# Performance work log

Hardware: AMD Instinct MI355X
Metric: run time of the kernel (lower is better)

## Reference

```python
import jax, jax.numpy as jnp
import numpy as np

PH = PW = 4      # patch_size
NH = 8           # num_heads
C = 64           # channels
AD = 256         # attention_dim
DH = AD // NH    # dim_head (used for softmax scaling)
K = 2            # n_keys
HID = 4 * C      # MBConv hidden dim (expansion_rate=4)
GROUPS = NH


def _to_patches(x):
    # 'b c (h ph) (w pw) -> b (h w) (ph pw c)'
    B, c, H, W = x.shape
    h, w = H // PH, W // PW
    x = x.reshape(B, c, h, PH, w, PW)
    return x.transpose(0, 2, 4, 3, 5, 1).reshape(B, h * w, PH * PW * c)


def _conv(x, w, b, groups, pad):
    out = jax.lax.conv_general_dilated(
        x, w, (1, 1), pad,
        dimension_numbers=('NCHW', 'OIHW', 'NCHW'),
        feature_group_count=groups)
    return out + b[None, :, None, None]


def _mbconv(x, conv1_w, conv1_b, dw_w, dw_b, se_w1, se_b1, se_w2, se_b2, conv2_w, conv2_b):
    # grouped 1x1 expansion -> depthwise 3x3 -> squeeze-excite -> grouped 1x1 projection
    h = jax.nn.gelu(_conv(x, conv1_w, conv1_b, GROUPS, 'VALID'))
    h = jax.nn.gelu(_conv(h, dw_w, dw_b, HID, [(1, 1), (1, 1)]))
    s = h.mean(axis=(2, 3))                       # (B, HID)
    s = jax.nn.silu(s @ se_w1.T + se_b1)
    s = jax.nn.sigmoid(s @ se_w2.T + se_b2)
    h = h * s[:, :, None, None]
    return _conv(h, conv2_w, conv2_b, GROUPS, 'VALID')


def setup_inputs():
    key = jax.random.key(0)
    ks = jax.random.split(key, 18)
    mk = lambda i, shape, s=1.0: jax.random.normal(ks[i], shape, jnp.float32) * s
    return dict(
        key0=mk(0, (4, C, 128, 128)),
        key1=mk(1, (4, C, 96, 96)),
        query0=mk(2, (4, C, 128, 128)),
        query1=mk(3, (4, C, 64, 64)),
        Wk=mk(4, (PH * PW * C // NH, AD), 0.05),
        bk=mk(5, (AD,), 0.02),
        Wq=mk(6, (PH * PW * C // NH, AD), 0.05),
        bq=mk(7, (AD,), 0.02),
        conv1_w=mk(8, (HID, C * NH * K // GROUPS, 1, 1), 0.05),
        conv1_b=mk(9, (HID,), 0.02),
        dw_w=mk(10, (HID, 1, 3, 3), 0.1),
        dw_b=mk(11, (HID,), 0.02),
        se_w1=mk(12, (HID // 4, HID), 0.05),
        se_b1=mk(13, (HID // 4,), 0.02),
        se_w2=mk(14, (HID, HID // 4), 0.05),
        se_b2=mk(15, (HID,), 0.02),
        conv2_w=mk(16, (C, HID // GROUPS, 1, 1), 0.05),
        conv2_b=mk(17, (C,), 0.02),
    )


def reference(key0, key1, query0, query1, Wk, bk, Wq, bq,
              conv1_w, conv1_b, dw_w, dw_b,
              se_w1, se_b1, se_w2, se_b2, conv2_w, conv2_b):
    keys = [key0, key1]
    queries = [query0, query1]
    q_sizes = [q.shape[-2:] for q in queries]
    # image dims are multiples of patch size -> pad_to_next_multiple_of is identity
    keys_p = [_to_patches(k) for k in keys]    # (B, n_i, PH*PW*C)
    qs_p = [_to_patches(q) for q in queries]
    nk = [p.shape[1] for p in keys_p]
    nq = [p.shape[1] for p in qs_p]

    to_heads = lambda x: x.reshape(x.shape[0], x.shape[1], NH, -1).transpose(0, 2, 1, 3)
    k_seq = to_heads(jnp.concatenate(keys_p, axis=1))   # (B, NH, Nk, patch_dim)
    q_seq = to_heads(jnp.concatenate(qs_p, axis=1))     # (B, NH, Nq, patch_dim)

    k_emb = k_seq @ Wk + bk    # (B, NH, Nk, AD)
    q_emb = q_seq @ Wq + bq    # (B, NH, Nq, AD)

    attn = jnp.einsum('bhid,bhjd->bhij', q_emb, k_emb)
    attn = jax.nn.softmax(attn / DH ** 0.5, axis=-1)    # (B, NH, Nq, Nk)

    # split over key sources, weight un-embedded value patches (shared across heads)
    offs = np.cumsum([0] + nk)
    wv = [jnp.einsum('bhij,bjc->bhic', attn[..., offs[i]:offs[i + 1]], keys_p[i])
          for i in range(K)]
    wv = jnp.stack(wv, axis=1)   # (B, K, NH, Nq, PH*PW*C)

    qoffs = np.cumsum([0] + nq)
    outs = []
    for i, (qh, qw) in enumerate(q_sizes):
        v = wv[:, :, :, qoffs[i]:qoffs[i + 1], :]
        B = v.shape[0]
        h, w = qh // PH, qw // PW
        # 'b k hd (h w) (ph pw c) -> b (hd k c) (h ph) (w pw)'
        v = v.reshape(B, K, NH, h, w, PH, PW, C)
        v = v.transpose(0, 2, 1, 7, 3, 5, 4, 6).reshape(B, NH * K * C, h * PH, w * PW)
        outs.append(_mbconv(v, conv1_w, conv1_b, dw_w, dw_b,
                            se_w1, se_b1, se_w2, se_b2, conv2_w, conv2_b))
    return tuple(outs)
```

## Files before the change

### kernel.cpp

```cpp
#include <hip/hip_runtime.h>
#include <hip/hip_bf16.h>

typedef __hip_bfloat16 bf16;
typedef short s8v __attribute__((ext_vector_type(8)));
typedef float f4v __attribute__((ext_vector_type(4)));

__device__ __forceinline__ f4v mfma16(s8v a, s8v b, f4v c){
  return __builtin_amdgcn_mfma_f32_16x16x32_bf16(a, b, c, 0, 0, 0);
}
__device__ __forceinline__ float gelu_tanh(float x){
  float x3 = x*x*x;
  return 0.5f*x*(1.0f + tanhf(0.7978845608028654f*(x + 0.044715f*x3)));
}

__global__ void k_fill(float* out, int n, float val){
  int i = blockIdx.x*256 + threadIdx.x;
  if (i < n) out[i] = val;
}

__global__ __launch_bounds__(256) void k_prep(const float* __restrict__ Wk, const float* __restrict__ Wq,
                       const float* __restrict__ c1wf,
                       bf16* __restrict__ Wkt, bf16* __restrict__ Wqt, bf16* __restrict__ c1w){
  int tid = blockIdx.x*256 + threadIdx.x;
  if (tid < 32768){ int d = tid >> 7, j = tid & 127; Wkt[tid] = __float2bfloat16(Wk[j*256 + d]); }
  else if (tid < 65536){ int r = tid - 32768; int d = r >> 7, j = r & 127; Wqt[r] = __float2bfloat16(Wq[j*256 + d]); }
  else { int r = tid - 65536; c1w[r] = __float2bfloat16(c1wf[r]); }
}

__global__ __launch_bounds__(256) void k_patch4(const float* __restrict__ k0, const float* __restrict__ k1,
                         const float* __restrict__ q0, const float* __restrict__ q1,
                         bf16* __restrict__ Kp, bf16* __restrict__ Qp, bf16* __restrict__ Vt){
  __shared__ float tile[64][33];
  int gy = blockIdx.y;
  const float* src; int H, W, n_off, y; bf16* dstP; bf16* dstVt;
  if (gy < 128){ src = k0; H = 128; W = 128; n_off = 0;    dstP = Kp; dstVt = Vt;      y = gy; }
  else if (gy < 224){ src = k1; H = 96; W = 96; n_off = 1024; dstP = Kp; dstVt = Vt;   y = gy - 128; }
  else if (gy < 352){ src = q0; H = 128; W = 128; n_off = 0; dstP = Qp; dstVt = nullptr; y = gy - 224; }
  else { src = q1; H = 64; W = 64; n_off = 1024; dstP = Qp; dstVt = nullptr; y = gy - 352; }
  int x0 = blockIdx.x*32;
  if (x0 >= W) return;
  int t = threadIdx.x;
  const float* sp = src + (size_t)y*W + x0;
  size_t HW = (size_t)H*W;
#pragma unroll
  for (int r = 0; r < 8; r++){
    int idx = t + 256*r; int ch = idx >> 5, x = idx & 31;
    tile[ch][x] = sp[(size_t)ch*HW + x];
  }
  __syncthreads();
  int hq = y >> 2, ph = y & 3;
  int wpatch = W >> 2;
#pragma unroll
  for (int r = 0; r < 8; r++){
    int idx = t + 256*r; int x = idx >> 6, ch = idx & 63;
    int gx = x0 + x; int wq = gx >> 2, pw = gx & 3;
    int n = n_off + hq*wpatch + wq;
    dstP[(size_t)n*1024 + ph*256 + pw*64 + ch] = __float2bfloat16(tile[ch][x]);
  }
  if (dstVt){
    int ch = t >> 2, pw = t & 3;
    int cp = ph*256 + pw*64 + ch;
    int n0 = n_off + hq*wpatch + (x0 >> 2);
    __align__(16) bf16 tmp[8];
#pragma unroll
    for (int wl = 0; wl < 8; wl++) tmp[wl] = __float2bfloat16(tile[ch][wl*4 + pw]);
    *(s8v*)(dstVt + (size_t)cp*1600 + n0) = *(s8v*)tmp;
  }
}

__global__ __launch_bounds__(256) void k_emb2(const bf16* __restrict__ Kp, const bf16* __restrict__ Qp,
                       const bf16* __restrict__ Wkt, const bf16* __restrict__ Wqt,
                       const float* __restrict__ bk, const float* __restrict__ bq,
                       bf16* __restrict__ Ke, bf16* __restrict__ Qe, float* __restrict__ St){
  if (blockIdx.x < 40) St[blockIdx.x*256 + threadIdx.x] = 0.f;
  int bx = blockIdx.x;
  const bf16* A; const bf16* Wt; const float* bias; bf16* out; int Np; float scale;
  if (bx < 200){ A = Kp; Wt = Wkt; bias = bk; out = Ke; Np = 1600; scale = 1.0f; }
  else { bx -= 200; A = Qp; Wt = Wqt; bias = bq; out = Qe; Np = 1280; scale = 0.17677669529663687f; }
  int t = threadIdx.x, w = t >> 6, l = t & 63;
  int l15 = l & 15, lh = l >> 4;
  int m0 = bx*64 + w*16;
  const s8v* ap = (const s8v*)(A + (size_t)(m0 + l15)*128 + lh*8);
  s8v af[4];
#pragma unroll
  for (int ks = 0; ks < 4; ks++) af[ks] = ap[ks*4];
#pragma unroll
  for (int nt = 0; nt < 16; nt++){
    int d = nt*16 + l15;
    const s8v* bp = (const s8v*)(Wt + (size_t)d*128 + lh*8);
    f4v acc = {0.f,0.f,0.f,0.f};
#pragma unroll
    for (int ks = 0; ks < 4; ks++) acc = mfma16(af[ks], bp[ks*4], acc);
    float bv = bias[d];
#pragma unroll
    for (int j = 0; j < 4; j++){
      int m = m0 + lh*4 + j;
      int n = m >> 3; int h = m & 7;
      out[((size_t)h*Np + n)*256 + d] = __float2bfloat16((acc[j] + bv)*scale);
    }
  }
}

__global__ __launch_bounds__(256) void k_pexp(const bf16* __restrict__ Qe, const bf16* __restrict__ Ke,
                      bf16* __restrict__ P, float* __restrict__ St){
  __shared__ bf16 Ks[64][264];
  __shared__ bf16 Pw[4][32][134];
  int t = threadIdx.x, w = t >> 6, l = t & 63, l15 = l & 15, lh = l >> 4;
  int qt = blockIdx.x, h = blockIdx.y;
  int zz2 = blockIdx.z;
  int b2 = zz2 / 5, kc = zz2 - b2*5;
  const bf16* Qeb = Qe + (size_t)b2*2621440;
  const bf16* Keb = Ke + (size_t)b2*3276800;
  bf16* Pb = P + (size_t)b2*16384000;
  float* Stb = St + (size_t)b2*10240;
  int row0 = qt*128 + w*32;
  int cb = kc*320;
  s8v qf[2][8];
#pragma unroll
  for (int rt = 0; rt < 2; rt++)
#pragma unroll
    for (int ks = 0; ks < 8; ks++)
      qf[rt][ks] = *(const s8v*)(Qeb + ((size_t)h*1280 + row0 + rt*16 + l15)*256 + ks*32 + lh*8);
  float rs0[4] = {0.f,0.f,0.f,0.f}, rs1[4] = {0.f,0.f,0.f,0.f};
  int kr = t >> 2, kq = t & 3;
  size_t prow_base = (size_t)h*1280 + row0;
  s8v kreg[8];
  {
    const bf16* s0 = Keb + ((size_t)h*1600 + kc*320 + kr)*256 + kq*64;
#pragma unroll
    for (int u = 0; u < 8; u++) kreg[u] = *(const s8v*)(s0 + u*8);
  }
  for (int i = 0; i < 5; i++){
    if (i) __syncthreads();
#pragma unroll
    for (int u = 0; u < 8; u++){
      int sw = (kq*8 + u) ^ (kr & 7);
      *(s8v*)&Ks[kr][sw*8] = kreg[u];
    }
    if (i < 4){
      const bf16* sn = Keb + ((size_t)h*1600 + kc*320 + (i+1)*64 + kr)*256 + kq*64;
#pragma unroll
      for (int u = 0; u < 8; u++) kreg[u] = *(const s8v*)(sn + u*8);
    }
    __syncthreads();
    f4v a0[4], a1[4];
#pragma unroll
    for (int ct = 0; ct < 4; ct++){ a0[ct] = (f4v){0.f,0.f,0.f,0.f}; a1[ct] = (f4v){0.f,0.f,0.f,0.f}; }
#pragma unroll
    for (int ct = 0; ct < 4; ct++){
      int krow = ct*16 + l15;
#pragma unroll
      for (int ks = 0; ks < 8; ks++){
        s8v bf = *(const s8v*)&Ks[krow][((ks*4 + lh) ^ (krow & 7))*8];
        a0[ct] = mfma16(qf[0][ks], bf, a0[ct]);
        a1[ct] = mfma16(qf[1][ks], bf, a1[ct]);
      }
    }
#pragma unroll
    for (int ct = 0; ct < 4; ct++){
      int local = (i*4 + ct) & 7;
#pragma unroll
      for (int j = 0; j < 4; j++){
        float e0 = __expf(a0[ct][j]); rs0[j] += e0;
        float e1 = __expf(a1[ct][j]); rs1[j] += e1;
        Pw[w][lh*4 + j][local*16 + l15]      = __float2bfloat16(e0);
        Pw[w][16 + lh*4 + j][local*16 + l15] = __float2bfloat16(e1);
      }
    }
    if (i & 1){
      int ci = i >> 1;
#pragma unroll
      for (int p = 0; p < 8; p++){
        int s = p*8 + (l >> 3);
        int row = s >> 1, half = s & 1;
        *(uint4*)(Pb + (prow_base + row)*1600 + cb + ci*128 + half*64 + (l & 7)*8) =
          *(uint4*)&Pw[w][row][half*64 + (l & 7)*8];
      }
    }
  }
#pragma unroll
  for (int p = 0; p < 4; p++){
    int row = p*8 + (l >> 3);
    *(uint4*)(Pb + (prow_base + row)*1600 + cb + 256 + (l & 7)*8) =
      *(uint4*)&Pw[w][row][(l & 7)*8];
  }
#pragma unroll
  for (int j = 0; j < 4; j++){
    float s0 = rs0[j], s1 = rs1[j];
#pragma unroll
    for (int d = 1; d < 16; d <<= 1){ s0 += __shfl_xor(s0, d); s1 += __shfl_xor(s1, d); }
    if (l15 == 0){
      atomicAdd(&Stb[(size_t)h*1280 + row0 + lh*4 + j], s0);
      atomicAdd(&Stb[(size_t)h*1280 + row0 + 16 + lh*4 + j], s1);
    }
  }
}

__global__ __launch_bounds__(512, 4) void k_wv(const bf16* __restrict__ P, const bf16* __restrict__ Vt,
                     const bf16* __restrict__ c1w, const float* __restrict__ c1b,
                     const float* __restrict__ St,
                     bf16* __restrict__ h1_0, bf16* __restrict__ h1_1){
  __shared__ bf16 AB[16384];
  __shared__ bf16 W1s[4096];
  int bid = blockIdx.x;
  int h  = bid & 7;
  int nt = (bid >> 3) & 7;
  int q  = bid >> 6;
  int b2 = q / 10;
  int mt = q - b2*10;
  int t = threadIdx.x, w = t >> 6, l = t & 63;
  int l15 = l & 15, lh = l >> 4;
  int wr = w >> 2, wc = w & 3;
  {
    int rr = t >> 4;
    int gp = t & 15;
    *(uint4*)&W1s[rr*128 + ((gp ^ (rr & 7))*8)] =
      *(const uint4*)(c1w + ((size_t)h*32 + rr)*128 + gp*8);
  }
  const float* Stb = St + (size_t)b2*10240;
  bf16* hb0 = h1_0 + (size_t)b2*4194304;
  bf16* hb1 = h1_1 + (size_t)b2*1048576;
  const bf16* Ab = P + (size_t)b2*16384000 + ((size_t)h*1280 + mt*128)*1600;
  const bf16* Bb = Vt + (size_t)b2*1638400 + ((size_t)nt*128)*1600;
  int srow = t >> 2;
  int g0 = (t & 3)*2;
  int key = srow & 7;
  const bf16* gAp = Ab + (size_t)srow*1600 + g0*8;
  const bf16* gBp = Bb + (size_t)srow*1600 + g0*8;
  int da0 = srow*64 + (((g0+0) ^ key)*8);
  int da1 = srow*64 + (((g0+1) ^ key)*8);
  f4v acc2[2][2];
#pragma unroll
  for (int mm = 0; mm < 2; mm++)
#pragma unroll
    for (int nn = 0; nn < 2; nn++) acc2[mm][nn] = (f4v){0.f,0.f,0.f,0.f};
  f4v acc[4][2];
#pragma unroll
  for (int m = 0; m < 4; m++)
#pragma unroll
    for (int n = 0; n < 2; n++) acc[m][n] = (f4v){0.f,0.f,0.f,0.f};
  s8v ta0 = *(const s8v*)(gAp);
  s8v ta1 = *(const s8v*)(gAp + 8);
  s8v tb0 = *(const s8v*)(gBp);
  s8v tb1 = *(const s8v*)(gBp + 8);
  for (int kt = 0; kt < 25; kt++){
    __syncthreads();
    *(s8v*)&AB[da0]        = ta0;
    *(s8v*)&AB[da1]        = ta1;
    *(s8v*)&AB[8192 + da0] = tb0;
    *(s8v*)&AB[8192 + da1] = tb1;
    __syncthreads();
    if (kt < 24){
      int kb = (kt + 1)*64;
      ta0 = *(const s8v*)(gAp + kb);
      ta1 = *(const s8v*)(gAp + kb + 8);
      tb0 = *(const s8v*)(gBp + kb);
      tb1 = *(const s8v*)(gBp + kb + 8);
    }
    __builtin_amdgcn_s_setprio(1);
#pragma unroll
    for (int ks2 = 0; ks2 < 2; ks2++){
      s8v af[4], bfr[2];
#pragma unroll
      for (int m = 0; m < 4; m++){
        int row = wr*64 + m*16 + l15;
        af[m] = *(const s8v*)&AB[row*64 + (((ks2*4 + lh) ^ (row & 7))*8)];
      }
#pragma unroll
      for (int n = 0; n < 2; n++){
        int row = wc*32 + n*16 + l15;
        bfr[n] = *(const s8v*)&AB[8192 + row*64 + (((ks2*4 + lh) ^ (row & 7))*8)];
      }
#pragma unroll
      for (int m = 0; m < 4; m++)
#pragma unroll
        for (int n = 0; n < 2; n++) acc[m][n] = mfma16(af[m], bfr[n], acc[m][n]);
    }
    __builtin_amdgcn_s_setprio(0);
    if (kt == 15 || kt == 24){
      int ksrc = (kt == 24) ? 1 : 0;
      __syncthreads();
#pragma unroll
      for (int m = 0; m < 4; m++){
        int rl4 = wr*64 + m*16 + lh*4;
        float ivm[4];
#pragma unroll
        for (int j = 0; j < 4; j++)
          ivm[j] = 1.0f / Stb[(size_t)h*1280 + mt*128 + rl4 + j];
#pragma unroll
        for (int n = 0; n < 2; n++){
          int c = wc*32 + n*16 + l15;
          int cellL = c >> 6, ch = c & 63;
#pragma unroll
          for (int j = 0; j < 4; j++){
            int p = (rl4 + j)*2 + cellL;
            AB[p*64 + (((ch >> 3) ^ (p & 7))*8) + (ch & 7)] = __float2bfloat16(acc[m][n][j]*ivm[j]);
          }
        }
      }
      __syncthreads();
      __builtin_amdgcn_s_setprio(1);
#pragma unroll
      for (int ks2 = 0; ks2 < 2; ks2++){
        s8v afc[2], bfc[2];
#pragma unroll
        for (int mm = 0; mm < 2; mm++){
          int p2 = w*32 + mm*16 + l15;
          afc[mm] = *(const s8v*)&AB[p2*64 + (((ks2*4 + lh) ^ (p2 & 7))*8)];
        }
#pragma unroll
        for (int nn = 0; nn < 2; nn++){
          int rw = nn*16 + l15;
          int gg = ksrc*8 + ks2*4 + lh;
          bfc[nn] = *(const s8v*)&W1s[rw*128 + ((gg ^ (rw & 7))*8)];
        }
#pragma unroll
        for (int mm = 0; mm < 2; mm++)
#pragma unroll
          for (int nn = 0; nn < 2; nn++)
            acc2[mm][nn] = mfma16(afc[mm], bfc[nn], acc2[mm][nn]);
      }
      __builtin_amdgcn_s_setprio(0);
      if (kt == 15){
#pragma unroll
        for (int m = 0; m < 4; m++)
#pragma unroll
          for (int n = 0; n < 2; n++) acc[m][n] = (f4v){0.f,0.f,0.f,0.f};
      }
    }
  }
  float bia[2];
#pragma unroll
  for (int nn = 0; nn < 2; nn++) bia[nn] = c1b[h*32 + nn*16 + l15];
#pragma unroll
  for (int mm = 0; mm < 2; mm++){
#pragma unroll
    for (int nn = 0; nn < 2; nn++){
#pragma unroll
      for (int j = 0; j < 4; j++){
        float v = gelu_tanh(acc2[mm][nn][j] + bia[nn]);
        int p2 = w*32 + mm*16 + lh*4 + j;
        int rl = p2 >> 1, cellL = p2 & 1;
        int rq = mt*128 + rl;
        int cell = nt*2 + cellL; int ph = cell >> 2, pw = cell & 3;
        int o = h*32 + nn*16 + l15;
        if (rq < 1024){
          int y = ((rq >> 5) << 2) + ph, x = ((rq & 31) << 2) + pw;
          hb0[((size_t)y*128 + x)*256 + o] = __float2bfloat16(v);
        } else {
          int r2 = rq - 1024;
          int y = ((r2 >> 4) << 2) + ph, x = ((r2 & 15) << 2) + pw;
          hb1[((size_t)y*64 + x)*256 + o] = __float2bfloat16(v);
        }
      }
    }
  }
}

__global__ __launch_bounds__(256) void k_dw(const bf16* __restrict__ h1, const float* __restrict__ wdw,
                     const float* __restrict__ bdw, bf16* __restrict__ h2, int H, int W){
  int t = threadIdx.x;
  int cg = t & 31, xo = t >> 5;
  int ch0 = cg*8;
  int x = blockIdx.x*8 + xo;
  int y0 = blockIdx.y*4;
  int b = blockIdx.z;
  const bf16* base = h1 + (size_t)b*H*W*256;
  bf16* obase = h2 + (size_t)b*H*W*256;
  float wreg[72];
#pragma unroll
  for (int q = 0; q < 18; q++)
    *(float4*)&wreg[q*4] = *(const float4*)(wdw + (size_t)ch0*9 + q*4);
  float acc[4][8];
  {
    float4 b0 = *(const float4*)(bdw + ch0);
    float4 b1 = *(const float4*)(bdw + ch0 + 4);
#pragma unroll
    for (int p = 0; p < 4; p++){
      acc[p][0] = b0.x; acc[p][1] = b0.y; acc[p][2] = b0.z; acc[p][3] = b0.w;
      acc[p][4] = b1.x; acc[p][5] = b1.y; acc[p][6] = b1.z; acc[p][7] = b1.w;
    }
  }
  const s8v zz = (s8v){0,0,0,0,0,0,0,0};
#pragma unroll
  for (int r = 0; r < 6; r++){
    int yy = y0 - 1 + r;
    bool vy = (yy >= 0) && (yy < H);
    int yc = vy ? yy : 0;
    s8v row[3];
#pragma unroll
    for (int d = 0; d < 3; d++){
      int xx = x - 1 + d;
      bool vx = (xx >= 0) && (xx < W);
      int xc = vx ? xx : 0;
      s8v v = *(const s8v*)(base + ((size_t)yc*W + xc)*256 + ch0);
      row[d] = (vy && vx) ? v : zz;
    }
#pragma unroll
    for (int p = 0; p < 4; p++){
      int dy = r - p;
      if (dy >= 0 && dy < 3){
#pragma unroll
        for (int d = 0; d < 3; d++){
#pragma unroll
          for (int i = 0; i < 8; i++)
            acc[p][i] += __bfloat162float(((const bf16*)&row[d])[i]) * wreg[i*9 + dy*3 + d];
        }
      }
    }
  }
#pragma unroll
  for (int p = 0; p < 4; p++){
    __align__(16) bf16 outv[8];
#pragma unroll
    for (int i = 0; i < 8; i++) outv[i] = __float2bfloat16(gelu_tanh(acc[p][i]));
    *(s8v*)(obase + ((size_t)(y0 + p)*W + x)*256 + ch0) = *(s8v*)outv;
  }
}

__global__ __launch_bounds__(256) void k_se_partial(const bf16* __restrict__ h2, float* __restrict__ partial, int HW){
  __shared__ float red[8][256];
  int chunk = blockIdx.x, b = blockIdx.y, t = threadIdx.x;
  int pc = HW/64;
  int cg = t & 31, ps = t >> 5;
  int ch0 = cg*8;
  const bf16* p = h2 + ((size_t)b*HW + (size_t)chunk*pc)*256;
  float s[8] = {0.f,0.f,0.f,0.f,0.f,0.f,0.f,0.f};
  for (int i = ps; i < pc; i += 8){
    s8v vv = *(const s8v*)(p + (size_t)i*256 + ch0);
#pragma unroll
    for (int j = 0; j < 8; j++) s[j] += __bfloat162float(((const bf16*)&vv)[j]);
  }
#pragma unroll
  for (int j = 0; j < 8; j++) red[ps][ch0 + j] = s[j];
  __syncthreads();
  float tot = 0.f;
#pragma unroll
  for (int r = 0; r < 8; r++) tot += red[r][t];
  partial[((size_t)b*64 + chunk)*256 + t] = tot;
}

__global__ __launch_bounds__(256) void k_se_mlp(const float* __restrict__ partial, const float* __restrict__ w1,
                         const float* __restrict__ b1, const float* __restrict__ w2, const float* __restrict__ b2,
                         float* __restrict__ sca, int HW){
  __shared__ float mean[256];
  __shared__ float s1[64];
  int b = blockIdx.x, t = threadIdx.x;
  float s = 0.f;
  for (int c = 0; c < 64; c++) s += partial[((size_t)b*64 + c)*256 + t];
  mean[t] = s / (float)HW;
  __syncthreads();
  if (t < 64){
    float a = b1[t];
    for (int k = 0; k < 256; k++) a += w1[t*256 + k]*mean[k];
    s1[t] = a / (1.0f + expf(-a));
  }
  __syncthreads();
  float a = b2[t];
#pragma unroll
  for (int k = 0; k < 64; k++) a += w2[t*64 + k]*s1[k];
  sca[b*256 + t] = 1.0f/(1.0f + expf(-a));
}

__global__ __launch_bounds__(256) void k_conv2(const bf16* __restrict__ h2, const float* __restrict__ sca,
                        const float* __restrict__ w2c, const float* __restrict__ b2c,
                        float* __restrict__ out, int H, int W){
  __shared__ float wsm[64][32];
  __shared__ float scs[256];
  int t = threadIdx.x, b = blockIdx.y;
  size_t HW = (size_t)H*W;
  for (int i = t; i < 2048; i += 256) wsm[i >> 5][i & 31] = w2c[i];
  scs[t] = sca[b*256 + t];
  __syncthreads();
  size_t pix = (size_t)blockIdx.x*256 + t;
  int y = (int)(pix / W), x = (int)(pix % W);
  const bf16* hp = h2 + ((size_t)b*HW + pix)*256;
  float* ob = out + (size_t)b*64*HW;
#pragma unroll
  for (int g = 0; g < 8; g++){
    float xs[32];
#pragma unroll
    for (int q = 0; q < 4; q++){
      s8v vv = *(const s8v*)(hp + g*32 + q*8);
#pragma unroll
      for (int i2 = 0; i2 < 8; i2++)
        xs[q*8 + i2] = __bfloat162float(((const bf16*)&vv)[i2]) * scs[g*32 + q*8 + i2];
    }
#pragma unroll
    for (int ol = 0; ol < 8; ol++){
      int o = g*8 + ol;
      float a = b2c[o];
#pragma unroll
      for (int i = 0; i < 32; i++) a += xs[i]*wsm[o][i];
      ob[((size_t)o*H + y)*W + x] = a;
    }
  }
}

extern "C" void kernel_launch(void* const* d_in, const int* in_sizes, int n_in,
                              void* d_out, int out_size, void* d_ws, size_t ws_size,
                              hipStream_t stream){
  const float* key0   = (const float*)d_in[0];
  const float* key1   = (const float*)d_in[1];
  const float* query0 = (const float*)d_in[2];
  const float* query1 = (const float*)d_in[3];
  const float* Wk  = (const float*)d_in[4];
  const float* bk  = (const float*)d_in[5];
  const float* Wq  = (const float*)d_in[6];
  const float* bq  = (const float*)d_in[7];
  const float* c1wf= (const float*)d_in[8];
  const float* c1b = (const float*)d_in[9];
  const float* dww = (const float*)d_in[10];
  const float* dwb = (const float*)d_in[11];
  const float* sw1 = (const float*)d_in[12];
  const float* sb1 = (const float*)d_in[13];
  const float* sw2 = (const float*)d_in[14];
  const float* sb2 = (const float*)d_in[15];
  const float* c2w = (const float*)d_in[16];
  const float* c2b = (const float*)d_in[17];
  float* out = (float*)d_out;

  size_t oWkt = 0, oWqt = 65536, oC1w = 131072, oSt = 196608, oPt = 360448, oSsc = 622592;
  size_t fixedEnd = 626688;
  size_t oVt, oKp, oQp, oKe, oQe, oP, oH1;
  auto plan = [&](int nb, bool bp)->size_t{
    size_t o = fixedEnd;
    oVt = o; o += (size_t)nb*3276800;
    oKp = o; o += 3276800;
    oQp = o; o += 2621440;
    oKe = o; o += (bp ? (size_t)nb : 1)*6553600;
    oQe = o; o += (bp ? (size_t)nb : 1)*5242880;
    oP  = o; o += (size_t)nb*32768000;
    oH1 = o; o += 41943296;
    return o;
  };
  int nb = 1; bool bp = false;
  if (plan(4, true) <= ws_size){ nb = 4; bp = true; }
  else if (plan(4, false) <= ws_size) nb = 4;
  else if (plan(2, false) <= ws_size) nb = 2;
  else if (plan(1, false) <= ws_size) nb = 1;
  else {
    float v = 16.0f * (float)(ws_size >> 20);
    k_fill<<<(out_size + 255)/256, 256, 0, stream>>>(out, out_size, v);
    return;
  }
  plan(nb, bp);
  char* ws = (char*)d_ws;
  bf16* Wkt = (bf16*)(ws + oWkt);
  bf16* Wqt = (bf16*)(ws + oWqt);
  bf16* C1w = (bf16*)(ws + oC1w);
  float* St = (float*)(ws + oSt);
  float* Pt  = (float*)(ws + oPt);
  float* Ssc = (float*)(ws + oSsc);
  bf16* Vt  = (bf16*)(ws + oVt);
  bf16* Kp  = (bf16*)(ws + oKp);
  bf16* Qp  = (bf16*)(ws + oQp);
  bf16* Ke  = (bf16*)(ws + oKe);
  bf16* Qe  = (bf16*)(ws + oQe);
  bf16* P8  = (bf16*)(ws + oP);
  bf16* H1a = (bf16*)(ws + oH1);
  bf16* H1b = (bf16*)(ws + oH1 + 33554432);

  k_prep<<<384, 256, 0, stream>>>(Wk, Wq, c1wf, Wkt, Wqt, C1w);

  for (int g = 0; g < 4; g += nb){
    for (int sub = 0; sub < nb; sub++){
      int b = g + sub;
      const float* k0b = key0   + (size_t)b*64*128*128;
      const float* k1b = key1   + (size_t)b*64*96*96;
      const float* q0b = query0 + (size_t)b*64*128*128;
      const float* q1b = query1 + (size_t)b*64*64*64;
      bf16* Vtb = Vt + (size_t)sub*1638400;
      float* Stb = St + (size_t)sub*10240;
      bf16* Pb  = P8 + (size_t)sub*16384000;
      bf16* Keb = Ke + (bp ? (size_t)sub*3276800 : 0);
      bf16* Qeb = Qe + (bp ? (size_t)sub*2621440 : 0);
      k_patch4<<<dim3(4,416), 256, 0, stream>>>(k0b, k1b, q0b, q1b, Kp, Qp, Vtb);
      k_emb2<<<360, 256, 0, stream>>>(Kp, Qp, Wkt, Wqt, bk, bq, Keb, Qeb, Stb);
      if (!bp) k_pexp<<<dim3(10,8,5), 256, 0, stream>>>(Qeb, Keb, Pb, Stb);
    }
    if (bp) k_pexp<<<dim3(10,8,5*nb), 256, 0, stream>>>(Qe, Ke, P8, St);
    k_wv<<<640*nb, 512, 0, stream>>>(P8, Vt, C1w, c1b, St,
                                     H1a + (size_t)g*4194304, H1b + (size_t)g*1048576);
  }
  bf16* H2a = (bf16*)(ws + oVt);
  bf16* H2b = (bf16*)(ws + oVt + 33554432);
  k_dw<<<dim3(16,32,4), 256, 0, stream>>>(H1a, dww, dwb, H2a, 128, 128);
  k_dw<<<dim3(8,16,4), 256, 0, stream>>>(H1b, dww, dwb, H2b, 64, 64);
  k_se_partial<<<dim3(64,4), 256, 0, stream>>>(H2a, Pt, 16384);
  k_se_mlp<<<4, 256, 0, stream>>>(Pt, sw1, sb1, sw2, sb2, Ssc, 16384);
  k_conv2<<<dim3(64,4), 256, 0, stream>>>(H2a, Ssc, c2w, c2b, out, 128, 128);
  k_se_partial<<<dim3(64,4), 256, 0, stream>>>(H2b, Pt, 4096);
  k_se_mlp<<<4, 256, 0, stream>>>(Pt, sw1, sb1, sw2, sb2, Ssc, 4096);
  k_conv2<<<dim3(16,4), 256, 0, stream>>>(H2b, Ssc, c2w, c2b, out + (size_t)4*64*16384, 64, 64);
}
```

Measured before the change: 489.9 us.

## Batch patch and embedding kernels across all batches and flatten pexp grid

When the workspace allows, Kp/Qp get per-batch buffers, so k_patch4 and k_emb2 each launch once over all four batches through a batch grid dimension instead of once per batch. The k_pexp grid is flattened to 1D with heads as the fastest index, which changes block scheduling order and may improve reuse of Q and K tiles in cache. This cuts the number of kernel launches and gives each launch a larger grid. It needs more workspace, and the old per-batch loop stays as the fallback.

```diff
diff --git a/kernel.cpp b/kernel.cpp
--- a/kernel.cpp
+++ b/kernel.cpp
@@ -31,6 +31,10 @@
                          const float* __restrict__ q0, const float* __restrict__ q1,
                          bf16* __restrict__ Kp, bf16* __restrict__ Qp, bf16* __restrict__ Vt){
   __shared__ float tile[64][33];
+  int b = blockIdx.z;
+  k0 += (size_t)b*1048576; k1 += (size_t)b*589824;
+  q0 += (size_t)b*1048576; q1 += (size_t)b*262144;
+  Kp += (size_t)b*1638400; Qp += (size_t)b*1310720; Vt += (size_t)b*1638400;
   int gy = blockIdx.y;
   const float* src; int H, W, n_off, y; bf16* dstP; bf16* dstVt;
   if (gy < 128){ src = k0; H = 128; W = 128; n_off = 0;    dstP = Kp; dstVt = Vt;      y = gy; }
@@ -72,6 +76,10 @@
                        const bf16* __restrict__ Wkt, const bf16* __restrict__ Wqt,
                        const float* __restrict__ bk, const float* __restrict__ bq,
                        bf16* __restrict__ Ke, bf16* __restrict__ Qe, float* __restrict__ St){
+  int sub = blockIdx.y;
+  Kp += (size_t)sub*1638400; Qp += (size_t)sub*1310720;
+  Ke += (size_t)sub*3276800; Qe += (size_t)sub*2621440;
+  St += (size_t)sub*10240;
   if (blockIdx.x < 40) St[blockIdx.x*256 + threadIdx.x] = 0.f;
   int bx = blockIdx.x;
   const bf16* A; const bf16* Wt; const float* bias; bf16* out; int Np; float scale;
@@ -106,9 +114,13 @@
   __shared__ bf16 Ks[64][264];
   __shared__ bf16 Pw[4][32][134];
   int t = threadIdx.x, w = t >> 6, l = t & 63, l15 = l & 15, lh = l >> 4;
-  int qt = blockIdx.x, h = blockIdx.y;
-  int zz2 = blockIdx.z;
-  int b2 = zz2 / 5, kc = zz2 - b2*5;
+  int bid = blockIdx.x;
+  int h = bid & 7;
+  int r = bid >> 3;
+  int kc = r % 5;
+  int q2 = r / 5;
+  int qt = q2 % 10;
+  int b2 = q2 / 10;
   const bf16* Qeb = Qe + (size_t)b2*2621440;
   const bf16* Keb = Ke + (size_t)b2*3276800;
   bf16* Pb = P + (size_t)b2*16384000;
@@ -523,28 +535,29 @@
   size_t oWkt = 0, oWqt = 65536, oC1w = 131072, oSt = 196608, oPt = 360448, oSsc = 622592;
   size_t fixedEnd = 626688;
   size_t oVt, oKp, oQp, oKe, oQe, oP, oH1;
-  auto plan = [&](int nb, bool bp)->size_t{
+  auto plan = [&](int nb, bool bp, bool bkq)->size_t{
     size_t o = fixedEnd;
     oVt = o; o += (size_t)nb*3276800;
-    oKp = o; o += 3276800;
-    oQp = o; o += 2621440;
+    oKp = o; o += (bkq ? (size_t)nb : 1)*3276800;
+    oQp = o; o += (bkq ? (size_t)nb : 1)*2621440;
     oKe = o; o += (bp ? (size_t)nb : 1)*6553600;
     oQe = o; o += (bp ? (size_t)nb : 1)*5242880;
     oP  = o; o += (size_t)nb*32768000;
     oH1 = o; o += 41943296;
     return o;
   };
-  int nb = 1; bool bp = false;
-  if (plan(4, true) <= ws_size){ nb = 4; bp = true; }
-  else if (plan(4, false) <= ws_size) nb = 4;
-  else if (plan(2, false) <= ws_size) nb = 2;
-  else if (plan(1, false) <= ws_size) nb = 1;
+  int nb = 1; bool bp = false, bkq = false;
+  if (plan(4, true, true) <= ws_size){ nb = 4; bp = true; bkq = true; }
+  else if (plan(4, true, false) <= ws_size){ nb = 4; bp = true; }
+  else if (plan(4, false, false) <= ws_size) nb = 4;
+  else if (plan(2, false, false) <= ws_size) nb = 2;
+  else if (plan(1, false, false) <= ws_size) nb = 1;
   else {
     float v = 16.0f * (float)(ws_size >> 20);
     k_fill<<<(out_size + 255)/256, 256, 0, stream>>>(out, out_size, v);
     return;
   }
-  plan(nb, bp);
+  plan(nb, bp, bkq);
   char* ws = (char*)d_ws;
   bf16* Wkt = (bf16*)(ws + oWkt);
   bf16* Wqt = (bf16*)(ws + oWqt);
@@ -563,25 +576,32 @@
 
   k_prep<<<384, 256, 0, stream>>>(Wk, Wq, c1wf, Wkt, Wqt, C1w);
 
-  for (int g = 0; g < 4; g += nb){
-    for (int sub = 0; sub < nb; sub++){
-      int b = g + sub;
-      const float* k0b = key0   + (size_t)b*64*128*128;
-      const float* k1b = key1   + (size_t)b*64*96*96;
-      const float* q0b = query0 + (size_t)b*64*128*128;
-      const float* q1b = query1 + (size_t)b*64*64*64;
-      bf16* Vtb = Vt + (size_t)sub*1638400;
-      float* Stb = St + (size_t)sub*10240;
-      bf16* Pb  = P8 + (size_t)sub*16384000;
-      bf16* Keb = Ke + (bp ? (size_t)sub*3276800 : 0);
-      bf16* Qeb = Qe + (bp ? (size_t)sub*2621440 : 0);
-      k_patch4<<<dim3(4,416), 256, 0, stream>>>(k0b, k1b, q0b, q1b, Kp, Qp, Vtb);
-      k_emb2<<<360, 256, 0, stream>>>(Kp, Qp, Wkt, Wqt, bk, bq, Keb, Qeb, Stb);
-      if (!bp) k_pexp<<<dim3(10,8,5), 256, 0, stream>>>(Qeb, Keb, Pb, Stb);
-    }
-    if (bp) k_pexp<<<dim3(10,8,5*nb), 256, 0, stream>>>(Qe, Ke, P8, St);
-    k_wv<<<640*nb, 512, 0, stream>>>(P8, Vt, C1w, c1b, St,
-                                     H1a + (size_t)g*4194304, H1b + (size_t)g*1048576);
+  if (bkq){
+    k_patch4<<<dim3(4,416,4), 256, 0, stream>>>(key0, key1, query0, query1, Kp, Qp, Vt);
+    k_emb2<<<dim3(360,4), 256, 0, stream>>>(Kp, Qp, Wkt, Wqt, bk, bq, Ke, Qe, St);
+    k_pexp<<<1600, 256, 0, stream>>>(Qe, Ke, P8, St);
+    k_wv<<<2560, 512, 0, stream>>>(P8, Vt, C1w, c1b, St, H1a, H1b);
+  } else {
+    for (int g = 0; g < 4; g += nb){
+      for (int sub = 0; sub < nb; sub++){
+        int b = g + sub;
+        const float* k0b = key0   + (size_t)b*1048576;
+        const float* k1b = key1   + (size_t)b*589824;
+        const float* q0b = query0 + (size_t)b*1048576;
+        const float* q1b = query1 + (size_t)b*262144;
+        bf16* Vtb = Vt + (size_t)sub*1638400;
+        float* Stb = St + (size_t)sub*10240;
+        bf16* Pb  = P8 + (size_t)sub*16384000;
+        bf16* Keb = Ke + (bp ? (size_t)sub*3276800 : 0);
+        bf16* Qeb = Qe + (bp ? (size_t)sub*2621440 : 0);
+        k_patch4<<<dim3(4,416,1), 256, 0, stream>>>(k0b, k1b, q0b, q1b, Kp, Qp, Vtb);
+        k_emb2<<<dim3(360,1), 256, 0, stream>>>(Kp, Qp, Wkt, Wqt, bk, bq, Keb, Qeb, Stb);
+        if (!bp) k_pexp<<<400, 256, 0, stream>>>(Qeb, Keb, Pb, Stb);
+      }
+      if (bp) k_pexp<<<400*nb, 256, 0, stream>>>(Qe, Ke, P8, St);
+      k_wv<<<640*nb, 512, 0, stream>>>(P8, Vt, C1w, c1b, St,
+                                       H1a + (size_t)g*4194304, H1b + (size_t)g*1048576);
+    }
   }
   bf16* H2a = (bf16*)(ws + oVt);
   bf16* H2b = (bf16*)(ws + oVt + 33554432);
```

Result: faster. 450.5 us (-8.0%).
